# Kernel tuning notes

Measured on AMD Instinct MI355X. Metric: run time of the kernel, lower is better.

The kernel has to match this reference:

```python
import jax, jax.numpy as jnp
import numpy as np

MAP_RANGE = 200.0


def setup_inputs() -> dict:
    key = jax.random.key(0)
    k1, k2 = jax.random.split(key)
    B, H, W, T, C = 4, 200, 200, 5, 64
    raw_bev_cache = jax.random.normal(k1, (B, H, W, T, C), dtype=jnp.float32)
    delta_ego_motion = jax.random.normal(k2, (B, 3), dtype=jnp.float32)
    return {"raw_bev_cache": raw_bev_cache, "delta_ego_motion": delta_ego_motion}


def _align_bev(raw_bev_cache, delta_ego_motion):
    B, H, W, T, C = raw_bev_cache.shape
    dtype = raw_bev_cache.dtype
    # --- theta (same math as torch code) ---
    dxn = delta_ego_motion[:, 0] / (MAP_RANGE / 2.0)
    dyn = delta_ego_motion[:, 1] / (MAP_RANGE / 2.0)
    dyaw = delta_ego_motion[:, 2]
    c = jnp.cos(dyaw)
    s = jnp.sin(dyaw)
    tx = -(c * dxn + s * dyn)
    ty = s * dxn - c * dyn
    # --- affine_grid, align_corners=False: normalized pixel-center coords ---
    xs = (2.0 * jnp.arange(W, dtype=dtype) + 1.0) / W - 1.0  # (W,)
    ys = (2.0 * jnp.arange(H, dtype=dtype) + 1.0) / H - 1.0  # (H,)
    # grid[b,h,w] = theta_b @ [x, y, 1]
    gx = c[:, None, None] * xs[None, None, :] + s[:, None, None] * ys[None, :, None] + tx[:, None, None]
    gy = -s[:, None, None] * xs[None, None, :] + c[:, None, None] * ys[None, :, None] + ty[:, None, None]
    # --- grid_sample: map normalized coords to source pixel coords (align_corners=False) ---
    ix = ((gx + 1.0) * W - 1.0) / 2.0  # (B,H,W)
    iy = ((gy + 1.0) * H - 1.0) / 2.0
    ix0f = jnp.floor(ix)
    iy0f = jnp.floor(iy)
    wx1 = ix - ix0f
    wx0 = 1.0 - wx1
    wy1 = iy - iy0f
    wy0 = 1.0 - wy1

    def corner(iyf, ixf):
        valid = (iyf >= 0) & (iyf <= H - 1) & (ixf >= 0) & (ixf <= W - 1)
        yi = jnp.clip(iyf, 0, H - 1).astype(jnp.int32)
        xi = jnp.clip(ixf, 0, W - 1).astype(jnp.int32)
        return yi, xi, valid.astype(dtype)

    y0, x0, m00 = corner(iy0f, ix0f)
    y0b, x1, m01 = corner(iy0f, ix0f + 1.0)
    y1, x0b, m10 = corner(iy0f + 1.0, ix0f)
    y1b, x1b, m11 = corner(iy0f + 1.0, ix0f + 1.0)

    # source frames to warp: (B, T-1, C, H, W)
    src = raw_bev_cache[:, :, :, : T - 1, :].transpose(0, 3, 4, 1, 2)

    gather = jax.vmap(lambda im, yi, xi: im[:, :, yi, xi])  # per-batch: (T-1,C,H,W)

    def bc(w):  # (B,H,W) -> (B,1,1,H,W)
        return w[:, None, None, :, :]

    out = (
        bc(wy0 * wx0 * m00) * gather(src, y0, x0)
        + bc(wy0 * wx1 * m01) * gather(src, y0b, x1)
        + bc(wy1 * wx0 * m10) * gather(src, y1, x0b)
        + bc(wy1 * wx1 * m11) * gather(src, y1b, x1b)
    )  # (B, T-1, C, H, W)

    transformed = out.transpose(0, 3, 4, 1, 2)  # (B,H,W,T-1,C)
    current = raw_bev_cache[:, :, :, T - 1 : T, :]
    return jnp.concatenate([transformed, current], axis=3)


def reference(raw_bev_cache, delta_ego_motion):
    return _align_bev(raw_bev_cache, delta_ego_motion)
```

## Files before the change

kernel.cpp:

```cpp
#include <hip/hip_runtime.h>
#include <math.h>

constexpr int Bn = 4, Hn = 200, Wn = 200, Tn = 5, Cn = 64;
constexpr int C4 = Cn / 4;
constexpr int TOTAL4 = Bn * Hn * Wn * Tn * C4;
constexpr int BLOCK = 256;

__global__ __launch_bounds__(BLOCK) void tf_warp_kernel(
    const float4* __restrict__ in4,
    const float*  __restrict__ ego,
    float4*       __restrict__ out4)
{
    int idx = blockIdx.x * BLOCK + threadIdx.x;

    int c4   = idx & (C4 - 1);
    int rest = idx >> 4;
    int t    = rest % Tn;
    int pos  = rest / Tn;
    int w    = pos % Wn;
    int bh   = pos / Wn;
    int h    = bh % Hn;
    int b    = bh / Hn;

    if (t == Tn - 1) {
        out4[idx] = in4[idx];
        return;
    }

    float dxn  = ego[b * 3 + 0] / 100.0f;
    float dyn  = ego[b * 3 + 1] / 100.0f;
    float dyaw = ego[b * 3 + 2];
    float sth, cth;
    sincosf(dyaw, &sth, &cth);
    float tx = -(cth * dxn + sth * dyn);
    float ty =  sth * dxn - cth * dyn;

    float xs = (2.0f * (float)w + 1.0f) / (float)Wn - 1.0f;
    float ys = (2.0f * (float)h + 1.0f) / (float)Hn - 1.0f;

    float gx =  cth * xs + sth * ys + tx;
    float gy = -sth * xs + cth * ys + ty;

    float ix = ((gx + 1.0f) * (float)Wn - 1.0f) * 0.5f;
    float iy = ((gy + 1.0f) * (float)Hn - 1.0f) * 0.5f;

    float ix0f = floorf(ix), iy0f = floorf(iy);
    float wx1 = ix - ix0f, wx0 = 1.0f - wx1;
    float wy1 = iy - iy0f, wy0 = 1.0f - wy1;
    float ix1f = ix0f + 1.0f, iy1f = iy0f + 1.0f;

    bool vx0 = (ix0f >= 0.0f) && (ix0f <= (float)(Wn - 1));
    bool vx1 = (ix1f >= 0.0f) && (ix1f <= (float)(Wn - 1));
    bool vy0 = (iy0f >= 0.0f) && (iy0f <= (float)(Hn - 1));
    bool vy1 = (iy1f >= 0.0f) && (iy1f <= (float)(Hn - 1));

    int x0 = (int)fminf(fmaxf(ix0f, 0.0f), (float)(Wn - 1));
    int x1 = (int)fminf(fmaxf(ix1f, 0.0f), (float)(Wn - 1));
    int y0 = (int)fminf(fmaxf(iy0f, 0.0f), (float)(Hn - 1));
    int y1 = (int)fminf(fmaxf(iy1f, 0.0f), (float)(Hn - 1));

    float w00 = wy0 * wx0 * ((vy0 && vx0) ? 1.0f : 0.0f);
    float w01 = wy0 * wx1 * ((vy0 && vx1) ? 1.0f : 0.0f);
    float w10 = wy1 * wx0 * ((vy1 && vx0) ? 1.0f : 0.0f);
    float w11 = wy1 * wx1 * ((vy1 && vx1) ? 1.0f : 0.0f);

    int bH = b * Hn;
    int i00 = (((bH + y0) * Wn + x0) * Tn + t) * C4 + c4;
    int i01 = (((bH + y0) * Wn + x1) * Tn + t) * C4 + c4;
    int i10 = (((bH + y1) * Wn + x0) * Tn + t) * C4 + c4;
    int i11 = (((bH + y1) * Wn + x1) * Tn + t) * C4 + c4;

    float4 v00 = in4[i00];
    float4 v01 = in4[i01];
    float4 v10 = in4[i10];
    float4 v11 = in4[i11];

    float4 o;
    o.x = w00 * v00.x + w01 * v01.x + w10 * v10.x + w11 * v11.x;
    o.y = w00 * v00.y + w01 * v01.y + w10 * v10.y + w11 * v11.y;
    o.z = w00 * v00.z + w01 * v01.z + w10 * v10.z + w11 * v11.z;
    o.w = w00 * v00.w + w01 * v01.w + w10 * v10.w + w11 * v11.w;
    out4[idx] = o;
}

extern "C" void kernel_launch(void* const* d_in, const int* in_sizes, int n_in,
                              void* d_out, int out_size, void* d_ws, size_t ws_size,
                              hipStream_t stream) {
    const float4* in4 = (const float4*)d_in[0];
    const float*  ego = (const float*)d_in[1];
    float4* out4 = (float4*)d_out;

    int grid = TOTAL4 / BLOCK;
    tf_warp_kernel<<<grid, BLOCK, 0, stream>>>(in4, ego, out4);
}
```

Before: 351.5 us.

## Compute bilinear sampling coords once per pixel and process all frames per thread

Each block now handles 16 output pixels. One thread per pixel computes the bilinear corner offsets and weights and shares them through LDS. Each thread then handles one channel quad across all five time slices, issuing 16 gathers plus one copy load before writing five outputs. This removes the sincos and coordinate math that was repeated for every (t, c4) element and gives each thread more loads in flight. In exchange it adds a block barrier, raises register pressure, and leaves most threads idle while the coordinates are computed.

```diff
diff --git a/kernel.cpp b/kernel.cpp
--- a/kernel.cpp
+++ b/kernel.cpp
@@ -3,84 +3,107 @@
 
 constexpr int Bn = 4, Hn = 200, Wn = 200, Tn = 5, Cn = 64;
 constexpr int C4 = Cn / 4;
-constexpr int TOTAL4 = Bn * Hn * Wn * Tn * C4;
-constexpr int BLOCK = 256;
+constexpr int PIXELS = Bn * Hn * Wn;
+constexpr int PPB = 16;
+constexpr int BLOCK = PPB * C4;
+constexpr int PIX_STRIDE4 = Tn * C4;
 
 __global__ __launch_bounds__(BLOCK) void tf_warp_kernel(
     const float4* __restrict__ in4,
     const float*  __restrict__ ego,
     float4*       __restrict__ out4)
 {
-    int idx = blockIdx.x * BLOCK + threadIdx.x;
+    __shared__ int   s_base[PPB][4];
+    __shared__ float s_wgt[PPB][4];
 
-    int c4   = idx & (C4 - 1);
-    int rest = idx >> 4;
-    int t    = rest % Tn;
-    int pos  = rest / Tn;
-    int w    = pos % Wn;
-    int bh   = pos / Wn;
-    int h    = bh % Hn;
-    int b    = bh / Hn;
+    const int tid  = threadIdx.x;
+    const int pos0 = blockIdx.x * PPB;
 
-    if (t == Tn - 1) {
-        out4[idx] = in4[idx];
-        return;
+    if (tid < PPB) {
+        int pos = pos0 + tid;
+        int w   = pos % Wn;
+        int bh  = pos / Wn;
+        int h   = bh % Hn;
+        int b   = bh / Hn;
+
+        float dxn  = ego[b * 3 + 0] * 0.01f;
+        float dyn  = ego[b * 3 + 1] * 0.01f;
+        float dyaw = ego[b * 3 + 2];
+        float sth, cth;
+        sincosf(dyaw, &sth, &cth);
+        float tx = -(cth * dxn + sth * dyn);
+        float ty =  sth * dxn - cth * dyn;
+
+        float xs = (2.0f * (float)w + 1.0f) / (float)Wn - 1.0f;
+        float ys = (2.0f * (float)h + 1.0f) / (float)Hn - 1.0f;
+
+        float gx =  cth * xs + sth * ys + tx;
+        float gy = -sth * xs + cth * ys + ty;
+
+        float ix = ((gx + 1.0f) * (float)Wn - 1.0f) * 0.5f;
+        float iy = ((gy + 1.0f) * (float)Hn - 1.0f) * 0.5f;
+
+        float ix0f = floorf(ix), iy0f = floorf(iy);
+        float wx1 = ix - ix0f, wx0 = 1.0f - wx1;
+        float wy1 = iy - iy0f, wy0 = 1.0f - wy1;
+        float ix1f = ix0f + 1.0f, iy1f = iy0f + 1.0f;
+
+        bool vx0 = (ix0f >= 0.0f) && (ix0f <= (float)(Wn - 1));
+        bool vx1 = (ix1f >= 0.0f) && (ix1f <= (float)(Wn - 1));
+        bool vy0 = (iy0f >= 0.0f) && (iy0f <= (float)(Hn - 1));
+        bool vy1 = (iy1f >= 0.0f) && (iy1f <= (float)(Hn - 1));
+
+        int x0 = (int)fminf(fmaxf(ix0f, 0.0f), (float)(Wn - 1));
+        int x1 = (int)fminf(fmaxf(ix1f, 0.0f), (float)(Wn - 1));
+        int y0 = (int)fminf(fmaxf(iy0f, 0.0f), (float)(Hn - 1));
+        int y1 = (int)fminf(fmaxf(iy1f, 0.0f), (float)(Hn - 1));
+
+        int bH = b * Hn;
+        s_base[tid][0] = ((bH + y0) * Wn + x0) * PIX_STRIDE4;
+        s_base[tid][1] = ((bH + y0) * Wn + x1) * PIX_STRIDE4;
+        s_base[tid][2] = ((bH + y1) * Wn + x0) * PIX_STRIDE4;
+        s_base[tid][3] = ((bH + y1) * Wn + x1) * PIX_STRIDE4;
+        s_wgt[tid][0]  = wy0 * wx0 * ((vy0 && vx0) ? 1.0f : 0.0f);
+        s_wgt[tid][1]  = wy0 * wx1 * ((vy0 && vx1) ? 1.0f : 0.0f);
+        s_wgt[tid][2]  = wy1 * wx0 * ((vy1 && vx0) ? 1.0f : 0.0f);
+        s_wgt[tid][3]  = wy1 * wx1 * ((vy1 && vx1) ? 1.0f : 0.0f);
     }
+    __syncthreads();
 
-    float dxn  = ego[b * 3 + 0] / 100.0f;
-    float dyn  = ego[b * 3 + 1] / 100.0f;
-    float dyaw = ego[b * 3 + 2];
-    float sth, cth;
-    sincosf(dyaw, &sth, &cth);
-    float tx = -(cth * dxn + sth * dyn);
-    float ty =  sth * dxn - cth * dyn;
+    const int p   = tid >> 4;
+    const int c4  = tid & (C4 - 1);
+    const int pos = pos0 + p;
+    const int obase = pos * PIX_STRIDE4 + c4;
 
-    float xs = (2.0f * (float)w + 1.0f) / (float)Wn - 1.0f;
-    float ys = (2.0f * (float)h + 1.0f) / (float)Hn - 1.0f;
+    const int b00 = s_base[p][0] + c4;
+    const int b01 = s_base[p][1] + c4;
+    const int b10 = s_base[p][2] + c4;
+    const int b11 = s_base[p][3] + c4;
+    const float w00 = s_wgt[p][0];
+    const float w01 = s_wgt[p][1];
+    const float w10 = s_wgt[p][2];
+    const float w11 = s_wgt[p][3];
 
-    float gx =  cth * xs + sth * ys + tx;
-    float gy = -sth * xs + cth * ys + ty;
+    float4 v00[4], v01[4], v10[4], v11[4];
+#pragma unroll
+    for (int t = 0; t < 4; ++t) {
+        v00[t] = in4[b00 + t * C4];
+        v01[t] = in4[b01 + t * C4];
+        v10[t] = in4[b10 + t * C4];
+        v11[t] = in4[b11 + t * C4];
+    }
+    float4 cur = in4[obase + 4 * C4];
 
-    float ix = ((gx + 1.0f) * (float)Wn - 1.0f) * 0.5f;
-    float iy = ((gy + 1.0f) * (float)Hn - 1.0f) * 0.5f;
-
-    float ix0f = floorf(ix), iy0f = floorf(iy);
-    float wx1 = ix - ix0f, wx0 = 1.0f - wx1;
-    float wy1 = iy - iy0f, wy0 = 1.0f - wy1;
-    float ix1f = ix0f + 1.0f, iy1f = iy0f + 1.0f;
-
-    bool vx0 = (ix0f >= 0.0f) && (ix0f <= (float)(Wn - 1));
-    bool vx1 = (ix1f >= 0.0f) && (ix1f <= (float)(Wn - 1));
-    bool vy0 = (iy0f >= 0.0f) && (iy0f <= (float)(Hn - 1));
-    bool vy1 = (iy1f >= 0.0f) && (iy1f <= (float)(Hn - 1));
-
-    int x0 = (int)fminf(fmaxf(ix0f, 0.0f), (float)(Wn - 1));
-    int x1 = (int)fminf(fmaxf(ix1f, 0.0f), (float)(Wn - 1));
-    int y0 = (int)fminf(fmaxf(iy0f, 0.0f), (float)(Hn - 1));
-    int y1 = (int)fminf(fmaxf(iy1f, 0.0f), (float)(Hn - 1));
-
-    float w00 = wy0 * wx0 * ((vy0 && vx0) ? 1.0f : 0.0f);
-    float w01 = wy0 * wx1 * ((vy0 && vx1) ? 1.0f : 0.0f);
-    float w10 = wy1 * wx0 * ((vy1 && vx0) ? 1.0f : 0.0f);
-    float w11 = wy1 * wx1 * ((vy1 && vx1) ? 1.0f : 0.0f);
-
-    int bH = b * Hn;
-    int i00 = (((bH + y0) * Wn + x0) * Tn + t) * C4 + c4;
-    int i01 = (((bH + y0) * Wn + x1) * Tn + t) * C4 + c4;
-    int i10 = (((bH + y1) * Wn + x0) * Tn + t) * C4 + c4;
-    int i11 = (((bH + y1) * Wn + x1) * Tn + t) * C4 + c4;
-
-    float4 v00 = in4[i00];
-    float4 v01 = in4[i01];
-    float4 v10 = in4[i10];
-    float4 v11 = in4[i11];
-
-    float4 o;
-    o.x = w00 * v00.x + w01 * v01.x + w10 * v10.x + w11 * v11.x;
-    o.y = w00 * v00.y + w01 * v01.y + w10 * v10.y + w11 * v11.y;
-    o.z = w00 * v00.z + w01 * v01.z + w10 * v10.z + w11 * v11.z;
-    o.w = w00 * v00.w + w01 * v01.w + w10 * v10.w + w11 * v11.w;
-    out4[idx] = o;
+#pragma unroll
+    for (int t = 0; t < 4; ++t) {
+        float4 o;
+        o.x = w00 * v00[t].x + w01 * v01[t].x + w10 * v10[t].x + w11 * v11[t].x;
+        o.y = w00 * v00[t].y + w01 * v01[t].y + w10 * v10[t].y + w11 * v11[t].y;
+        o.z = w00 * v00[t].z + w01 * v01[t].z + w10 * v10[t].z + w11 * v11[t].z;
+        o.w = w00 * v00[t].w + w01 * v01[t].w + w10 * v10[t].w + w11 * v11[t].w;
+        out4[obase + t * C4] = o;
+    }
+    out4[obase + 4 * C4] = cur;
 }
 
 extern "C" void kernel_launch(void* const* d_in, const int* in_sizes, int n_in,
@@ -90,6 +113,6 @@
     const float*  ego = (const float*)d_in[1];
     float4* out4 = (float4*)d_out;
 
-    int grid = TOTAL4 / BLOCK;
+    int grid = PIXELS / PPB;
     tf_warp_kernel<<<grid, BLOCK, 0, stream>>>(in4, ego, out4);
 }
```

After: 342.0 us. 2.7% less time.
